# Performance work log

Hardware: AMD Instinct MI355X
Metric: run time of the kernel (lower is better)

The kernel has to match this reference:

```python
import jax, jax.numpy as jnp
import numpy as np

B, S, DIM = 2, 2048, 2048
N_HEADS = 16
KV_LORA = 512
NOPE_D = 128
ROPE_D = 64
V_D = 128
Q_D = NOPE_D + ROPE_D  # 192
EPS = 1e-6


def _make_rope_cache(seqlen, head_dim):
    # [cos | sin] layout per position, GPT-NeoX half-rotation convention
    half = head_dim // 2
    inv_freq = 1.0 / (10000.0 ** (np.arange(0, half, dtype=np.float32) / half))
    t = np.arange(seqlen, dtype=np.float32)
    freqs = np.outer(t, inv_freq)                    # [S, half]
    emb = np.concatenate([freqs, freqs], axis=-1)    # [S, head_dim]
    return jnp.asarray(np.concatenate([np.cos(emb), np.sin(emb)], axis=-1))  # [S, 2*head_dim]


def setup_inputs() -> dict:
    key = jax.random.key(0)
    ks = jax.random.split(key, 6)
    x = jax.random.normal(ks[0], (B, S, DIM), dtype=jnp.float32)
    rope_cache = _make_rope_cache(S, ROPE_D)         # [S, 128]
    std = 0.02
    wq = jax.random.normal(ks[1], (N_HEADS * Q_D, DIM), dtype=jnp.float32) * std
    wkva = jax.random.normal(ks[2], (KV_LORA + ROPE_D, DIM), dtype=jnp.float32) * std
    norm_w = jnp.ones((KV_LORA,), dtype=jnp.float32)
    wkvb = jax.random.normal(ks[3], (N_HEADS * (NOPE_D + V_D), KV_LORA), dtype=jnp.float32) * std
    wo = jax.random.normal(ks[4], (DIM, N_HEADS * V_D), dtype=jnp.float32) * std
    return {"x": x, "rope_cache": rope_cache, "wq": wq, "wkva": wkva,
            "norm_w": norm_w, "wkvb": wkvb, "wo": wo}


def _rotate_half(t):
    h = t.shape[-1] // 2
    return jnp.concatenate([-t[..., h:], t[..., :h]], axis=-1)


def _rms_norm(t, w):
    tf = t.astype(jnp.float32)
    y = tf * jax.lax.rsqrt(jnp.mean(tf * tf, axis=-1, keepdims=True) + EPS)
    return (y * w).astype(t.dtype)


def reference(x, rope_cache, wq, wkva, norm_w, wkvb, wo):
    bs, seqlen, _ = x.shape
    scale = Q_D ** (-0.5)

    q = (x @ wq.T).reshape(bs, seqlen, N_HEADS, Q_D)
    q_nope, q_rope = q[..., :NOPE_D], q[..., NOPE_D:]

    ckv = x @ wkva.T                                 # [b,s,KV_LORA+ROPE_D]
    kv_pass, k_rope = ckv[..., :KV_LORA], ckv[..., KV_LORA:]
    kv = (_rms_norm(kv_pass, norm_w) @ wkvb.T).reshape(bs, seqlen, N_HEADS, NOPE_D + V_D)
    k_nope, v = kv[..., :NOPE_D], kv[..., NOPE_D:]

    k_rope = jnp.broadcast_to(k_rope[:, :, None, :], (bs, seqlen, N_HEADS, ROPE_D))

    cos = rope_cache[:seqlen, :ROPE_D][None, :, None, :]
    sin = rope_cache[:seqlen, ROPE_D:2 * ROPE_D][None, :, None, :]
    q_rope = q_rope * cos + _rotate_half(q_rope) * sin
    k_rope = k_rope * cos + _rotate_half(k_rope) * sin

    qf = jnp.concatenate([q_nope, q_rope], axis=-1)  # [b,s,h,192]
    kf = jnp.concatenate([k_nope, k_rope], axis=-1)

    # causal SDPA
    scores = jnp.einsum('bqhd,bkhd->bhqk', qf, kf) * scale
    mask = jnp.tril(jnp.ones((seqlen, seqlen), dtype=bool))
    scores = jnp.where(mask, scores, jnp.finfo(scores.dtype).min)
    probs = jax.nn.softmax(scores, axis=-1)
    out = jnp.einsum('bhqk,bkhd->bqhd', probs, v).reshape(bs, seqlen, N_HEADS * V_D)
    return out @ wo.T
```

## Files before the change

### kernel.cpp

```cpp
#include <hip/hip_runtime.h>
#include <cstdint>
#include <cstddef>

#define B_      2
#define S_      2048
#define DIM_    2048
#define H_      16
#define KV_LORA_ 512
#define NOPE_D_ 128
#define ROPE_D_ 64
#define V_D_    128
#define Q_D_    192
#define EPS_    1e-6f
#define BS_     (B_ * S_)
#define CKV_P_  768

typedef __attribute__((ext_vector_type(8))) short bf16x8;
typedef __attribute__((ext_vector_type(4))) float f32x4;
typedef __attribute__((ext_vector_type(16))) float f32x16;

__device__ __forceinline__ ushort f2bf(float f) {
    union { float f; uint32_t u; } v; v.f = f;
    uint32_t u = v.u + 0x7fff + ((v.u >> 16) & 1);
    return (ushort)(u >> 16);
}
__device__ __forceinline__ float bf2f(ushort u) {
    union { uint32_t u; float f; } v; v.u = (uint32_t)u << 16; return v.f;
}
__device__ __forceinline__ void gll16(const void* g, void* l) {
    __builtin_amdgcn_global_load_lds(
        (const __attribute__((address_space(1))) unsigned int*)g,
        (__attribute__((address_space(3))) unsigned int*)l, 16, 0, 0);
}

#define GQ_BARRIER()  __builtin_amdgcn_s_barrier()
#define GQ_LGKM0()    do { asm volatile("s_waitcnt lgkmcnt(0)" ::: "memory"); \
                           __builtin_amdgcn_sched_barrier(0); } while (0)

template <int MODE>
__global__ __launch_bounds__(512, 2) void gemm256_8ph(
    const ushort* __restrict__ A, const ushort* __restrict__ Bw,
    void* __restrict__ Cv, void* __restrict__ Cv2, int N, int K, int nbx)
{
    __shared__ __align__(16) ushort L[2][2][2][4][256][8];

    const int tid = threadIdx.x;
    const int lane = tid & 63;
    const int w = tid >> 6;
    const int l15 = lane & 15, quad = lane >> 4;

    const int nwg = (int)gridDim.x;
    const int cpx = nwg >> 3;
    const int lin = (int)blockIdx.x;
    const int swz = (lin & 7) * cpx + (lin >> 3);
    const int m0 = (swz / nbx) * 256;
    const int n0 = (swz % nbx) * 256;

    const int wm0 = (w & 3) * 64;
    const int wn0 = (w >> 2) * 128;

    const int NT = K >> 6;

    f32x4 acc[4][8];
#pragma unroll
    for (int i = 0; i < 4; ++i)
#pragma unroll
        for (int j = 0; j < 8; ++j) acc[i][j] = (f32x4){0.f, 0.f, 0.f, 0.f};

    auto stage = [&](int ab, int kh, int kt, int buf) {
#pragma unroll
        for (int j = 0; j < 2; ++j) {
            int ci = w + j * 8;
            int qd = ci >> 2, rg = ci & 3;
            ushort* dst = &L[buf][ab][kh][qd][rg * 64 + lane][0];
            const ushort* src = (ab ? Bw + (size_t)(n0 + rg * 64 + lane) * K
                                    : A  + (size_t)(m0 + rg * 64 + lane) * K)
                                + kt * 64 + kh * 32 + qd * 8;
            gll16(src, dst);
        }
    };

    stage(0, 0, 0, 0); stage(1, 0, 0, 0); stage(0, 1, 0, 0); stage(1, 1, 0, 0);
    if (NT > 1) { stage(0, 0, 1, 1); stage(1, 0, 1, 1); stage(0, 1, 1, 1); }
    else        { stage(0, 0, 0, 1); stage(1, 0, 0, 1); stage(0, 1, 0, 1); }
    asm volatile("s_waitcnt vmcnt(6)" ::: "memory");
    GQ_BARRIER();

    bf16x8 a[4], b[4];

    for (int t = 0; t < NT; ++t) {
        const int c = t & 1, o = c ^ 1;
        const int kt1 = (t + 1 < NT) ? t + 1 : 0;
        const int kt2 = (t + 2 < NT) ? t + 2 : 0;

#pragma unroll
        for (int fm = 0; fm < 4; ++fm)
            a[fm] = *(const bf16x8*)&L[c][0][0][quad][wm0 + fm * 16 + l15][0];
#pragma unroll
        for (int fn = 0; fn < 4; ++fn)
            b[fn] = *(const bf16x8*)&L[c][1][0][quad][wn0 + fn * 16 + l15][0];
        stage(1, 1, kt1, o);
        GQ_BARRIER();
        GQ_LGKM0();
        __builtin_amdgcn_s_setprio(1);
#pragma unroll
        for (int fm = 0; fm < 4; ++fm)
#pragma unroll
            for (int fn = 0; fn < 4; ++fn)
                acc[fm][fn] = __builtin_amdgcn_mfma_f32_16x16x32_bf16(a[fm], b[fn], acc[fm][fn], 0, 0, 0);
        __builtin_amdgcn_s_setprio(0);
        GQ_BARRIER();

#pragma unroll
        for (int fn = 0; fn < 4; ++fn)
            b[fn] = *(const bf16x8*)&L[c][1][0][quad][wn0 + 64 + fn * 16 + l15][0];
        stage(0, 0, kt2, c);
        GQ_BARRIER();
        GQ_LGKM0();
        __builtin_amdgcn_s_setprio(1);
#pragma unroll
        for (int fm = 0; fm < 4; ++fm)
#pragma unroll
            for (int fn = 0; fn < 4; ++fn)
                acc[fm][4 + fn] = __builtin_amdgcn_mfma_f32_16x16x32_bf16(a[fm], b[fn], acc[fm][4 + fn], 0, 0, 0);
        __builtin_amdgcn_s_setprio(0);
        GQ_BARRIER();

#pragma unroll
        for (int fm = 0; fm < 4; ++fm)
            a[fm] = *(const bf16x8*)&L[c][0][1][quad][wm0 + fm * 16 + l15][0];
#pragma unroll
        for (int fn = 0; fn < 4; ++fn)
            b[fn] = *(const bf16x8*)&L[c][1][1][quad][wn0 + fn * 16 + l15][0];
        stage(1, 0, kt2, c);
        GQ_BARRIER();
        GQ_LGKM0();
        __builtin_amdgcn_s_setprio(1);
#pragma unroll
        for (int fm = 0; fm < 4; ++fm)
#pragma unroll
            for (int fn = 0; fn < 4; ++fn)
                acc[fm][fn] = __builtin_amdgcn_mfma_f32_16x16x32_bf16(a[fm], b[fn], acc[fm][fn], 0, 0, 0);
        __builtin_amdgcn_s_setprio(0);
        GQ_BARRIER();

#pragma unroll
        for (int fn = 0; fn < 4; ++fn)
            b[fn] = *(const bf16x8*)&L[c][1][1][quad][wn0 + 64 + fn * 16 + l15][0];
        stage(0, 1, kt2, c);
        GQ_BARRIER();
        GQ_LGKM0();
        __builtin_amdgcn_s_setprio(1);
#pragma unroll
        for (int fm = 0; fm < 4; ++fm)
#pragma unroll
            for (int fn = 0; fn < 4; ++fn)
                acc[fm][4 + fn] = __builtin_amdgcn_mfma_f32_16x16x32_bf16(a[fm], b[fn], acc[fm][4 + fn], 0, 0, 0);
        __builtin_amdgcn_s_setprio(0);
        asm volatile("s_waitcnt vmcnt(6)" ::: "memory");
        GQ_BARRIER();
    }

#pragma unroll
    for (int fm = 0; fm < 4; ++fm)
#pragma unroll
        for (int r = 0; r < 4; ++r) {
            int row = m0 + wm0 + fm * 16 + quad * 4 + r;
            if (MODE == 2) {
                if (n0 < 3072) {
                    size_t base = (size_t)row * 3072 + n0 + wn0 + l15;
#pragma unroll
                    for (int fn = 0; fn < 8; ++fn)
                        ((ushort*)Cv)[base + fn * 16] = f2bf(acc[fm][fn][r]);
                } else {
                    size_t base = (size_t)row * CKV_P_ + (n0 - 3072) + wn0 + l15;
#pragma unroll
                    for (int fn = 0; fn < 8; ++fn)
                        ((float*)Cv2)[base + fn * 16] = acc[fm][fn][r];
                }
            } else {
                size_t base = (size_t)row * N + n0 + wn0 + l15;
#pragma unroll
                for (int fn = 0; fn < 8; ++fn) {
                    float v = acc[fm][fn][r];
                    if (MODE == 1) ((ushort*)Cv)[base + fn * 16] = f2bf(v);
                    else           ((float*)Cv)[base + fn * 16] = v;
                }
            }
        }
}

template <int OUT_BF16>
__global__ __launch_bounds__(512, 2) void gemm_bn128(
    const ushort* __restrict__ A, const ushort* __restrict__ Bw,
    void* __restrict__ Cv, int N, int K, int nbx)
{
    __shared__ __align__(16) ushort LA[2][2][4][256][8];
    __shared__ __align__(16) ushort LB[2][2][4][128][8];

    const int tid = threadIdx.x;
    const int lane = tid & 63;
    const int w = tid >> 6;
    const int l15 = lane & 15, quad = lane >> 4;

    const int nwg = (int)gridDim.x;
    const int cpx = nwg >> 3;
    const int lin = (int)blockIdx.x;
    const int swz = (lin & 7) * cpx + (lin >> 3);
    const int m0 = (swz / nbx) * 256;
    const int n0 = (swz % nbx) * 128;

    const int wm0 = (w & 3) * 64;
    const int wn0 = (w >> 2) * 64;

    const int NT = K >> 6;

    f32x4 acc[4][4];
#pragma unroll
    for (int i = 0; i < 4; ++i)
#pragma unroll
        for (int j = 0; j < 4; ++j) acc[i][j] = (f32x4){0.f, 0.f, 0.f, 0.f};

    auto stageA = [&](int kh, int kt, int buf) {
#pragma unroll
        for (int j = 0; j < 2; ++j) {
            int ci = w + j * 8;
            int qd = ci >> 2, rg = ci & 3;
            ushort* dst = &LA[buf][kh][qd][rg * 64 + lane][0];
            const ushort* src = A + (size_t)(m0 + rg * 64 + lane) * K
                                + kt * 64 + kh * 32 + qd * 8;
            gll16(src, dst);
        }
    };
    auto stageB = [&](int kt, int buf) {
#pragma unroll
        for (int j = 0; j < 2; ++j) {
            int ci = w + j * 8;
            int kh = ci >> 3, qd = (ci >> 1) & 3, rh = ci & 1;
            ushort* dst = &LB[buf][kh][qd][rh * 64 + lane][0];
            const ushort* src = Bw + (size_t)(n0 + rh * 64 + lane) * K
                                + kt * 64 + kh * 32 + qd * 8;
            gll16(src, dst);
        }
    };

    stageA(0, 0, 0); stageA(1, 0, 0); stageB(0, 0);
    stageA(0, (NT > 1) ? 1 : 0, 1);
    asm volatile("s_waitcnt vmcnt(2)" ::: "memory");
    GQ_BARRIER();

    bf16x8 a[4], b[4];

    for (int t = 0; t < NT; ++t) {
        const int c = t & 1, o = c ^ 1;
        const int kt1 = (t + 1 < NT) ? t + 1 : 0;
        const int kt2 = (t + 2 < NT) ? t + 2 : 0;

#pragma unroll
        for (int fm = 0; fm < 4; ++fm)
            a[fm] = *(const bf16x8*)&LA[c][0][quad][wm0 + fm * 16 + l15][0];
#pragma unroll
        for (int fn = 0; fn < 4; ++fn)
            b[fn] = *(const bf16x8*)&LB[c][0][quad][wn0 + fn * 16 + l15][0];
        stageA(1, kt1, o); stageB(kt1, o);
        GQ_BARRIER();
        GQ_LGKM0();
        __builtin_amdgcn_s_setprio(1);
#pragma unroll
        for (int fm = 0; fm < 4; ++fm)
#pragma unroll
            for (int fn = 0; fn < 4; ++fn)
                acc[fm][fn] = __builtin_amdgcn_mfma_f32_16x16x32_bf16(a[fm], b[fn], acc[fm][fn], 0, 0, 0);
        __builtin_amdgcn_s_setprio(0);
        GQ_BARRIER();

#pragma unroll
        for (int fm = 0; fm < 4; ++fm)
            a[fm] = *(const bf16x8*)&LA[c][1][quad][wm0 + fm * 16 + l15][0];
#pragma unroll
        for (int fn = 0; fn < 4; ++fn)
            b[fn] = *(const bf16x8*)&LB[c][1][quad][wn0 + fn * 16 + l15][0];
        stageA(0, kt2, c);
        GQ_BARRIER();
        GQ_LGKM0();
        __builtin_amdgcn_s_setprio(1);
#pragma unroll
        for (int fm = 0; fm < 4; ++fm)
#pragma unroll
            for (int fn = 0; fn < 4; ++fn)
                acc[fm][fn] = __builtin_amdgcn_mfma_f32_16x16x32_bf16(a[fm], b[fn], acc[fm][fn], 0, 0, 0);
        __builtin_amdgcn_s_setprio(0);
        asm volatile("s_waitcnt vmcnt(2)" ::: "memory");
        GQ_BARRIER();
    }

#pragma unroll
    for (int fm = 0; fm < 4; ++fm)
#pragma unroll
        for (int r = 0; r < 4; ++r) {
            size_t base = (size_t)(m0 + wm0 + fm * 16 + quad * 4 + r) * N + n0 + wn0 + l15;
#pragma unroll
            for (int fn = 0; fn < 4; ++fn) {
                float v = acc[fm][fn][r];
                if (OUT_BF16) ((ushort*)Cv)[base + fn * 16] = f2bf(v);
                else          ((float*)Cv)[base + fn * 16] = v;
            }
        }
}

__global__ __launch_bounds__(256) void cast_all(
    const float* __restrict__ x, const float* __restrict__ wq,
    const float* __restrict__ wkva, const float* __restrict__ wkvb,
    const float* __restrict__ wo,
    ushort* __restrict__ xb, ushort* __restrict__ wc,
    ushort* __restrict__ wkvb_bf, ushort* __restrict__ wo_bf)
{
    size_t i = ((size_t)blockIdx.x * 256 + threadIdx.x) * 8;
    const float* s; ushort* d;
    if (i < 8388608)        { s = x + i;                  d = xb + i; }
    else if (i < 14680064)  { s = wq + (i - 8388608);     d = wc + (i - 8388608); }
    else if (i < 15859712)  { s = wkva + (i - 14680064);  d = wc + (i - 8388608); }
    else if (i < 16252928)  {
        ushort4 z = {0, 0, 0, 0};
        ushort* dz = wc + (i - 8388608);
        *(ushort4*)dz = z; *(ushort4*)(dz + 4) = z;
        return;
    }
    else if (i < 18350080)  { s = wkvb + (i - 16252928);  d = wkvb_bf + (i - 16252928); }
    else                    { s = wo + (i - 18350080);    d = wo_bf + (i - 18350080); }
    float4 a = *(const float4*)s;
    float4 b = *(const float4*)(s + 4);
    ushort4 o0, o1;
    o0.x = f2bf(a.x); o0.y = f2bf(a.y); o0.z = f2bf(a.z); o0.w = f2bf(a.w);
    o1.x = f2bf(b.x); o1.y = f2bf(b.y); o1.z = f2bf(b.z); o1.w = f2bf(b.w);
    *(ushort4*)d = o0;
    *(ushort4*)(d + 4) = o1;
}

__global__ __launch_bounds__(256) void rmsnorm_rope_k(
    const float* __restrict__ ckv, const float* __restrict__ nw,
    const float* __restrict__ rope_cache,
    ushort* __restrict__ cnorm, ushort* __restrict__ krb)
{
    const int lane = threadIdx.x & 63;
    const int row = blockIdx.x * 4 + (threadIdx.x >> 6);
    const float* src = ckv + (size_t)row * CKV_P_;
    float4 a = *(const float4*)(src + lane * 4);
    float4 b = *(const float4*)(src + 256 + lane * 4);
    float ss = a.x*a.x + a.y*a.y + a.z*a.z + a.w*a.w
             + b.x*b.x + b.y*b.y + b.z*b.z + b.w*b.w;
#pragma unroll
    for (int off = 32; off > 0; off >>= 1) ss += __shfl_xor(ss, off, 64);
    float rs = rsqrtf(ss * (1.0f / 512.0f) + EPS_);
    float4 w0 = *(const float4*)(nw + lane * 4);
    float4 w1 = *(const float4*)(nw + 256 + lane * 4);
    ushort* dst = cnorm + (size_t)row * KV_LORA_;
    ushort4 o0, o1;
    o0.x = f2bf(a.x*rs*w0.x); o0.y = f2bf(a.y*rs*w0.y);
    o0.z = f2bf(a.z*rs*w0.z); o0.w = f2bf(a.w*rs*w0.w);
    o1.x = f2bf(b.x*rs*w1.x); o1.y = f2bf(b.y*rs*w1.y);
    o1.z = f2bf(b.z*rs*w1.z); o1.w = f2bf(b.w*rs*w1.w);
    *(ushort4*)(dst + lane * 4) = o0;
    *(ushort4*)(dst + 256 + lane * 4) = o1;

    float v = src[KV_LORA_ + lane];
    float other = __shfl_xor(v, 32, 64);
    float rot = (lane < 32) ? -other : other;
    int s = row & (S_ - 1);
    float c  = rope_cache[s * (2 * ROPE_D_) + lane];
    float sn = rope_cache[s * (2 * ROPE_D_) + ROPE_D_ + lane];
    krb[(size_t)row * ROPE_D_ + lane] = f2bf(v * c + rot * sn);
}

__global__ __launch_bounds__(256) void rope_q_inplace(
    ushort* __restrict__ q_bf, const float* __restrict__ rope_cache)
{
    const int lane = threadIdx.x & 63;
    const int wv = blockIdx.x * 4 + (threadIdx.x >> 6);
    const int bsr = wv >> 4;
    const int h = wv & 15;
    const int s = bsr & (S_ - 1);
    ushort* p = q_bf + (size_t)bsr * (H_ * Q_D_) + h * Q_D_ + 128;
    float v = bf2f(p[lane]);
    float other = __shfl_xor(v, 32, 64);
    float rot = (lane < 32) ? -other : other;
    float c  = rope_cache[s * (2 * ROPE_D_) + lane];
    float sn = rope_cache[s * (2 * ROPE_D_) + ROPE_D_ + lane];
    p[lane] = f2bf(v * c + rot * sn);
}

__global__ __launch_bounds__(256) void transpose_v(
    const ushort* __restrict__ kvb, ushort* __restrict__ vT)
{
    __shared__ ushort T[128][80];
    const int tid = threadIdx.x;
    const int bh = blockIdx.y;
    const int b = bh >> 4, h = bh & 15;
    const int sb = blockIdx.x * 64;
    const size_t rowbase = (size_t)b * S_ + sb;
#pragma unroll
    for (int it = 0; it < 4; ++it) {
        int f = tid + 256 * it;
        int r = f >> 4, c8 = (f & 15) * 8;
        bf16x8 v = *(const bf16x8*)(kvb + (rowbase + r) * 4096 + h * 256 + 128 + c8);
#pragma unroll
        for (int e = 0; e < 8; ++e) T[c8 + e][r] = (ushort)v[e];
    }
    __syncthreads();
#pragma unroll
    for (int it = 0; it < 4; ++it) {
        int f = tid + 256 * it;
        int vd = f >> 3, s8 = (f & 7) * 8;
        *(bf16x8*)(vT + ((size_t)bh * 128 + vd) * S_ + sb + s8) =
            *(const bf16x8*)&T[vd][s8];
    }
}

__global__ __launch_bounds__(512, 2) void mla_attn_mfma5(
    const ushort* __restrict__ qb, const ushort* __restrict__ kvb,
    const ushort* __restrict__ krb, const ushort* __restrict__ vT,
    ushort* __restrict__ attn)
{
    __shared__ __align__(16) ushort LDSU[40960];
    const int KFo[2] = {0, 12288};
    const int VFo[2] = {24576, 32768};

    const int tid = threadIdx.x;
    const int lane = tid & 63;
    const int w = tid >> 6;
    const int l31 = lane & 31, hi = lane >> 5;
    const int band = w & 3;
    const int koff = (w >> 2) * 32;

    const int lin = (int)blockIdx.y * 8 + (int)blockIdx.x;
    const int swz = (lin & 7) * 32 + (lin >> 3);
    const int bh = swz >> 3;
    const int px = swz & 7;
    const int b = bh >> 4, h = bh & 15;
    const size_t bS = (size_t)b * S_;
    const float scale = 0.07216878364870323f;

    auto stage = [&](int kbase, int bufi) {
#pragma unroll
        for (int r = 0; r < 3; ++r) {
            int c = w + r * 8;
            ushort* dst = &LDSU[KFo[bufi] + (c * 64 + lane) * 8];
            const ushort* src = (c < 16)
                ? kvb + (bS + kbase + lane) * 4096 + h * 256 + c * 8
                : krb + (bS + kbase + lane) * 64 + (c - 16) * 8;
            gll16(src, dst);
        }
#pragma unroll
        for (int r = 0; r < 2; ++r) {
            int c = w + r * 8;
            ushort* dst = &LDSU[VFo[bufi] + (((c & 7) * 128) + (c >> 3) * 64 + lane) * 8];
            const ushort* src =
                vT + ((size_t)bh * 128 + (c >> 3) * 64 + lane) * S_ + kbase + (c & 7) * 8;
            gll16(src, dst);
        }
    };

#pragma unroll 1
    for (int hv = 0; hv < 2; ++hv) {
        const int qt = hv ? 15 - px : px;
        const int qbase = qt * 128;
        const int nkt = 2 * qt + 2;
        const int bmin = qbase + band * 32;

        stage(0, 0);

        bf16x8 qf[12];
        {
            const ushort* qrow = qb + (bS + bmin + l31) * (size_t)(H_ * Q_D_) + h * Q_D_;
#pragma unroll
            for (int c = 0; c < 12; ++c)
                qf[c] = *(const bf16x8*)(qrow + c * 16 + hi * 8);
        }

        f32x16 ov[4];
#pragma unroll
        for (int vt = 0; vt < 4; ++vt)
#pragma unroll
            for (int r = 0; r < 16; ++r) ov[vt][r] = 0.f;
        float m_run = -3e38f, lsum = 0.f;

        __syncthreads();

        for (int kt = 0; kt < nkt; ++kt) {
            const int kb = kt * 64;
            const int cur = kt & 1;
            if (kt + 1 < nkt) stage((kt + 1) * 64, cur ^ 1);

            const int kg = kb + koff;
            if (kg <= bmin + 31) {
                f32x16 sc;
#pragma unroll
                for (int r = 0; r < 16; ++r) sc[r] = 0.f;
                __builtin_amdgcn_s_setprio(1);
#pragma unroll
                for (int c = 0; c < 12; ++c) {
                    bf16x8 kf = *(const bf16x8*)
                        &LDSU[KFo[cur] + ((c * 2 + hi) * 64 + koff + l31) * 8];
                    sc = __builtin_amdgcn_mfma_f32_32x32x16_bf16(kf, qf[c], sc, 0, 0, 0);
                }
                __builtin_amdgcn_s_setprio(0);

                const bool need_mask = (kg == bmin);
                float p[16]; float mx = -3e38f;
#pragma unroll
                for (int r = 0; r < 16; ++r) {
                    float v = sc[r] * scale;
                    if (need_mask) {
                        int kr = (r & 3) + 8 * (r >> 2) + 4 * hi;
                        if (kr > l31) v = -3e38f;
                    }
                    p[r] = v; mx = fmaxf(mx, v);
                }
                mx = fmaxf(mx, __shfl_xor(mx, 32, 64));
                if (!__all(mx - m_run <= 8.0f)) {
                    float mn = fmaxf(mx, m_run);
                    float al = __expf(m_run - mn);
                    m_run = mn; lsum *= al;
#pragma unroll
                    for (int vt = 0; vt < 4; ++vt)
#pragma unroll
                        for (int r = 0; r < 16; ++r) ov[vt][r] *= al;
                }
                float s_loc = 0.f;
#pragma unroll
                for (int r = 0; r < 16; ++r) { p[r] = __expf(p[r] - m_run); s_loc += p[r]; }
                lsum += s_loc + __shfl_xor(s_loc, 32, 64);

                uint32_t w8[8];
#pragma unroll
                for (int m = 0; m < 8; ++m)
                    w8[m] = (uint32_t)f2bf(p[2 * m]) | ((uint32_t)f2bf(p[2 * m + 1]) << 16);
                bf16x8 pb[2];
#pragma unroll
                for (int c = 0; c < 2; ++c) {
                    uint32_t wd[4];
#pragma unroll
                    for (int par = 0; par < 2; ++par) {
                        uint32_t a  = w8[4 * c + par];
                        uint32_t bb = w8[4 * c + 2 + par];
                        uint32_t t  = __shfl_xor(bb, 32, 64);
                        uint32_t t2 = __shfl_xor(a, 32, 64);
                        wd[par]     = hi ? t : a;
                        wd[par + 2] = hi ? bb : t2;
                    }
                    union { uint32_t u[4]; bf16x8 v; } cvt;
                    cvt.u[0] = wd[0]; cvt.u[1] = wd[1]; cvt.u[2] = wd[2]; cvt.u[3] = wd[3];
                    pb[c] = cvt.v;
                }

                __builtin_amdgcn_s_setprio(1);
#pragma unroll
                for (int vt = 0; vt < 4; ++vt)
#pragma unroll
                    for (int c = 0; c < 2; ++c) {
                        bf16x8 vf = *(const bf16x8*)
                            &LDSU[VFo[cur] + (((koff >> 3) + c * 2 + hi) * 128 + vt * 32 + l31) * 8];
                        ov[vt] = __builtin_amdgcn_mfma_f32_32x32x16_bf16(vf, pb[c], ov[vt], 0, 0, 0);
                    }
                __builtin_amdgcn_s_setprio(0);
            }
            __syncthreads();
        }

        float* mrg = (float*)LDSU;
        if (w >= 4) {
            float* dst = mrg + (size_t)((w - 4) * 64 + lane) * 68;
#pragma unroll
            for (int vt = 0; vt < 4; ++vt)
#pragma unroll
                for (int g = 0; g < 4; ++g) {
                    f32x4 v4v = { ov[vt][g * 4 + 0], ov[vt][g * 4 + 1],
                                  ov[vt][g * 4 + 2], ov[vt][g * 4 + 3] };
                    *(f32x4*)(dst + vt * 16 + g * 4) = v4v;
                }
            dst[64] = m_run; dst[65] = lsum;
        }
        __syncthreads();
        if (w < 4) {
            const float* srcm = mrg + (size_t)(w * 64 + lane) * 68;
            float mB = srcm[64], lB = srcm[65];
            float M = fmaxf(m_run, mB);
            float eA = __expf(m_run - M), eB = __expf(mB - M);
            float L = lsum * eA + lB * eB;
            float inv = 1.0f / L;
            size_t obase = (bS + bmin + l31) * (size_t)(H_ * V_D_) + h * V_D_;
#pragma unroll
            for (int vt = 0; vt < 4; ++vt)
#pragma unroll
                for (int g = 0; g < 4; ++g) {
                    ushort4 o;
                    o.x = f2bf((ov[vt][g*4+0] * eA + srcm[vt*16+g*4+0] * eB) * inv);
                    o.y = f2bf((ov[vt][g*4+1] * eA + srcm[vt*16+g*4+1] * eB) * inv);
                    o.z = f2bf((ov[vt][g*4+2] * eA + srcm[vt*16+g*4+2] * eB) * inv);
                    o.w = f2bf((ov[vt][g*4+3] * eA + srcm[vt*16+g*4+3] * eB) * inv);
                    *(ushort4*)(attn + obase + vt * 32 + g * 8 + hi * 4) = o;
                }
        }
        __syncthreads();
    }
}

extern "C" void kernel_launch(void* const* d_in, const int* in_sizes, int n_in,
                              void* d_out, int out_size, void* d_ws, size_t ws_size,
                              hipStream_t stream)
{
    const float* x          = (const float*)d_in[0];
    const float* rope_cache = (const float*)d_in[1];
    const float* wq         = (const float*)d_in[2];
    const float* wkva       = (const float*)d_in[3];
    const float* norm_w     = (const float*)d_in[4];
    const float* wkvb       = (const float*)d_in[5];
    const float* wo         = (const float*)d_in[6];
    float* out = (float*)d_out;

    char* p = (char*)d_ws;
    ushort* xb       = (ushort*)p; p += (size_t)BS_ * DIM_ * 2;
    ushort* q_bf     = (ushort*)p; p += (size_t)BS_ * H_ * Q_D_ * 2;
    float*  ckv      = (float*) p; p += (size_t)BS_ * CKV_P_ * 4;
    ushort* cnorm_bf = (ushort*)p; p += (size_t)BS_ * KV_LORA_ * 2;
    ushort* kvb      = (ushort*)p; p += (size_t)BS_ * 4096 * 2;
    ushort* attn_bf  = (ushort*)p; p += (size_t)BS_ * 2048 * 2;
    ushort* krb      = (ushort*)p; p += (size_t)BS_ * ROPE_D_ * 2;
    ushort* wc_bf    = (ushort*)p; p += (size_t)3840 * DIM_ * 2;
    ushort* wkvb_bf  = (ushort*)p; p += (size_t)4096 * KV_LORA_ * 2;
    ushort* wo_bf    = (ushort*)p; p += (size_t)DIM_ * 2048 * 2;
    ushort* vT       = xb;

    cast_all<<<11008, dim3(256), 0, stream>>>(
        x, wq, wkva, wkvb, wo, xb, wc_bf, wkvb_bf, wo_bf);

    gemm256_8ph<2><<<dim3(16 * 15), dim3(512), 0, stream>>>(
        xb, wc_bf, q_bf, ckv, 0, DIM_, 15);
    rmsnorm_rope_k<<<BS_ / 4, dim3(256), 0, stream>>>(
        ckv, norm_w, rope_cache, cnorm_bf, krb);
    rope_q_inplace<<<BS_ * H_ / 4, dim3(256), 0, stream>>>(q_bf, rope_cache);
    gemm256_8ph<1><<<dim3(16 * 16), dim3(512), 0, stream>>>(
        cnorm_bf, wkvb_bf, kvb, nullptr, 4096, KV_LORA_, 16);
    transpose_v<<<dim3(S_ / 64, B_ * H_), dim3(256), 0, stream>>>(kvb, vT);
    mla_attn_mfma5<<<dim3(8, B_ * H_), dim3(512), 0, stream>>>(
        q_bf, kvb, krb, vT, attn_bf);
    gemm_bn128<0><<<dim3(16 * 16), dim3(512), 0, stream>>>(
        attn_bf, wo_bf, out, 2048, 2048, 16);
}
```

Measured before the change: 417.3 us.

## Fuse V transpose into kv_b GEMM epilogue and Q RoPE into attention

Adds a GEMM epilogue mode in which half the waves write K-nope rows directly and the other half transpose their V tile through LDS and write it into the vT layout. This removes the separate transpose_v kernel. The rope_q_inplace kernel is also removed: the attention kernel now applies the rotary embedding to the Q rope fragments in registers while loading them. Two launches and their global round trips go away, in exchange for extra epilogue work, LDS reuse in the GEMM, and some register pressure in attention. The GEMM also no longer writes the V half of kvb, so correctness depends on attention reading V only from vT.

```diff
diff --git a/kernel.cpp b/kernel.cpp
--- a/kernel.cpp
+++ b/kernel.cpp
@@ -161,6 +161,50 @@
         GQ_BARRIER();
     }
 
+    if (MODE == 3) {
+        asm volatile("s_waitcnt vmcnt(0)" ::: "memory");
+        GQ_BARRIER();
+        const int h = n0 >> 8;
+        if (w < 4) {
+#pragma unroll
+            for (int fm = 0; fm < 4; ++fm)
+#pragma unroll
+                for (int r = 0; r < 4; ++r) {
+                    size_t base = (size_t)(m0 + wm0 + fm * 16 + quad * 4 + r) * 4096
+                                  + n0 + wn0 + l15;
+#pragma unroll
+                    for (int fn = 0; fn < 8; ++fn)
+                        ((ushort*)Cv)[base + fn * 16] = f2bf(acc[fm][fn][r]);
+                }
+        } else {
+            ushort* T = &L[0][0][0][0][0][0] + (size_t)(w - 4) * (128 * 80);
+#pragma unroll
+            for (int fm = 0; fm < 4; ++fm)
+#pragma unroll
+                for (int fn = 0; fn < 8; ++fn) {
+                    uint32_t lo = (uint32_t)f2bf(acc[fm][fn][0])
+                                | ((uint32_t)f2bf(acc[fm][fn][1]) << 16);
+                    uint32_t hi2 = (uint32_t)f2bf(acc[fm][fn][2])
+                                 | ((uint32_t)f2bf(acc[fm][fn][3]) << 16);
+                    uint2 pk; pk.x = lo; pk.y = hi2;
+                    *(uint2*)&T[(size_t)(fn * 16 + l15) * 80 + fm * 16 + quad * 4] = pk;
+                }
+            asm volatile("s_waitcnt lgkmcnt(0)" ::: "memory");
+            __builtin_amdgcn_sched_barrier(0);
+            const int bh = (m0 >> 11) * 16 + h;
+            const int sbase = (m0 & 2047) + (w & 3) * 64;
+            ushort* vT = (ushort*)Cv2;
+#pragma unroll
+            for (int j = 0; j < 16; ++j) {
+                int cc = j * 64 + lane;
+                int vd = cc >> 3;
+                int s8 = (cc & 7) * 8;
+                bf16x8 v = *(const bf16x8*)&T[(size_t)vd * 80 + s8];
+                *(bf16x8*)(vT + ((size_t)bh * 128 + vd) * 2048 + sbase + s8) = v;
+            }
+        }
+        return;
+    }
 #pragma unroll
     for (int fm = 0; fm < 4; ++fm)
 #pragma unroll
@@ -372,54 +416,10 @@
     krb[(size_t)row * ROPE_D_ + lane] = f2bf(v * c + rot * sn);
 }
 
-__global__ __launch_bounds__(256) void rope_q_inplace(
-    ushort* __restrict__ q_bf, const float* __restrict__ rope_cache)
-{
-    const int lane = threadIdx.x & 63;
-    const int wv = blockIdx.x * 4 + (threadIdx.x >> 6);
-    const int bsr = wv >> 4;
-    const int h = wv & 15;
-    const int s = bsr & (S_ - 1);
-    ushort* p = q_bf + (size_t)bsr * (H_ * Q_D_) + h * Q_D_ + 128;
-    float v = bf2f(p[lane]);
-    float other = __shfl_xor(v, 32, 64);
-    float rot = (lane < 32) ? -other : other;
-    float c  = rope_cache[s * (2 * ROPE_D_) + lane];
-    float sn = rope_cache[s * (2 * ROPE_D_) + ROPE_D_ + lane];
-    p[lane] = f2bf(v * c + rot * sn);
-}
-
-__global__ __launch_bounds__(256) void transpose_v(
-    const ushort* __restrict__ kvb, ushort* __restrict__ vT)
-{
-    __shared__ ushort T[128][80];
-    const int tid = threadIdx.x;
-    const int bh = blockIdx.y;
-    const int b = bh >> 4, h = bh & 15;
-    const int sb = blockIdx.x * 64;
-    const size_t rowbase = (size_t)b * S_ + sb;
-#pragma unroll
-    for (int it = 0; it < 4; ++it) {
-        int f = tid + 256 * it;
-        int r = f >> 4, c8 = (f & 15) * 8;
-        bf16x8 v = *(const bf16x8*)(kvb + (rowbase + r) * 4096 + h * 256 + 128 + c8);
-#pragma unroll
-        for (int e = 0; e < 8; ++e) T[c8 + e][r] = (ushort)v[e];
-    }
-    __syncthreads();
-#pragma unroll
-    for (int it = 0; it < 4; ++it) {
-        int f = tid + 256 * it;
-        int vd = f >> 3, s8 = (f & 7) * 8;
-        *(bf16x8*)(vT + ((size_t)bh * 128 + vd) * S_ + sb + s8) =
-            *(const bf16x8*)&T[vd][s8];
-    }
-}
-
-__global__ __launch_bounds__(512, 2) void mla_attn_mfma5(
+__global__ __launch_bounds__(512, 2) void mla_attn_mfma6(
     const ushort* __restrict__ qb, const ushort* __restrict__ kvb,
     const ushort* __restrict__ krb, const ushort* __restrict__ vT,
-    ushort* __restrict__ attn)
+    const float* __restrict__ rope_cache, ushort* __restrict__ attn)
 {
     __shared__ __align__(16) ushort LDSU[40960];
     const int KFo[2] = {0, 12288};
@@ -473,8 +473,38 @@
         {
             const ushort* qrow = qb + (bS + bmin + l31) * (size_t)(H_ * Q_D_) + h * Q_D_;
 #pragma unroll
-            for (int c = 0; c < 12; ++c)
+            for (int c = 0; c < 8; ++c)
                 qf[c] = *(const bf16x8*)(qrow + c * 16 + hi * 8);
+            bf16x8 q8  = *(const bf16x8*)(qrow + 128 + hi * 8);
+            bf16x8 q9  = *(const bf16x8*)(qrow + 144 + hi * 8);
+            bf16x8 q10 = *(const bf16x8*)(qrow + 160 + hi * 8);
+            bf16x8 q11 = *(const bf16x8*)(qrow + 176 + hi * 8);
+            const float* rc = rope_cache + (size_t)(bmin + l31) * 128 + hi * 8;
+            f32x4 c8a = *(const f32x4*)(rc + 0),  c8b = *(const f32x4*)(rc + 4);
+            f32x4 c9a = *(const f32x4*)(rc + 16), c9b = *(const f32x4*)(rc + 20);
+            f32x4 cAa = *(const f32x4*)(rc + 32), cAb = *(const f32x4*)(rc + 36);
+            f32x4 cBa = *(const f32x4*)(rc + 48), cBb = *(const f32x4*)(rc + 52);
+            f32x4 s8a = *(const f32x4*)(rc + 64), s8b = *(const f32x4*)(rc + 68);
+            f32x4 s9a = *(const f32x4*)(rc + 80), s9b = *(const f32x4*)(rc + 84);
+            f32x4 sAa = *(const f32x4*)(rc + 96), sAb = *(const f32x4*)(rc + 100);
+            f32x4 sBa = *(const f32x4*)(rc + 112), sBb = *(const f32x4*)(rc + 116);
+            bf16x8 o8, o9, o10, o11;
+#pragma unroll
+            for (int e = 0; e < 4; ++e) {
+                float a8 = bf2f((ushort)q8[e]),  b8 = bf2f((ushort)q8[e + 4]);
+                float a9 = bf2f((ushort)q9[e]),  b9 = bf2f((ushort)q9[e + 4]);
+                float aA = bf2f((ushort)q10[e]), bA = bf2f((ushort)q10[e + 4]);
+                float aB = bf2f((ushort)q11[e]), bB = bf2f((ushort)q11[e + 4]);
+                o8[e]      = (short)f2bf(a8 * c8a[e] - aA * s8a[e]);
+                o8[e + 4]  = (short)f2bf(b8 * c8b[e] - bA * s8b[e]);
+                o9[e]      = (short)f2bf(a9 * c9a[e] - aB * s9a[e]);
+                o9[e + 4]  = (short)f2bf(b9 * c9b[e] - bB * s9b[e]);
+                o10[e]     = (short)f2bf(aA * cAa[e] + a8 * sAa[e]);
+                o10[e + 4] = (short)f2bf(bA * cAb[e] + b8 * sAb[e]);
+                o11[e]     = (short)f2bf(aB * cBa[e] + a9 * sBa[e]);
+                o11[e + 4] = (short)f2bf(bB * cBb[e] + b9 * sBb[e]);
+            }
+            qf[8] = o8; qf[9] = o9; qf[10] = o10; qf[11] = o11;
         }
 
         f32x16 ov[4];
@@ -638,12 +668,10 @@
         xb, wc_bf, q_bf, ckv, 0, DIM_, 15);
     rmsnorm_rope_k<<<BS_ / 4, dim3(256), 0, stream>>>(
         ckv, norm_w, rope_cache, cnorm_bf, krb);
-    rope_q_inplace<<<BS_ * H_ / 4, dim3(256), 0, stream>>>(q_bf, rope_cache);
-    gemm256_8ph<1><<<dim3(16 * 16), dim3(512), 0, stream>>>(
-        cnorm_bf, wkvb_bf, kvb, nullptr, 4096, KV_LORA_, 16);
-    transpose_v<<<dim3(S_ / 64, B_ * H_), dim3(256), 0, stream>>>(kvb, vT);
-    mla_attn_mfma5<<<dim3(8, B_ * H_), dim3(512), 0, stream>>>(
-        q_bf, kvb, krb, vT, attn_bf);
+    gemm256_8ph<3><<<dim3(16 * 16), dim3(512), 0, stream>>>(
+        cnorm_bf, wkvb_bf, kvb, vT, 4096, KV_LORA_, 16);
+    mla_attn_mfma6<<<dim3(8, B_ * H_), dim3(512), 0, stream>>>(
+        q_bf, kvb, krb, vT, rope_cache, attn_bf);
     gemm_bn128<0><<<dim3(16 * 16), dim3(512), 0, stream>>>(
         attn_bf, wo_bf, out, 2048, 2048, 16);
 }
```

After: 409.3 us. No clear change (-1.9%).
